# Kernel tuning notes

Measured on AMD Instinct MI355X. Metric: run time of the kernel, lower is better.

## Reference

```python
import jax, jax.numpy as jnp
import numpy as np

B, DIM_IN, DIM_OUT = 8192, 2048, 512


def setup_inputs() -> dict:
    key = jax.random.key(0)
    k1, k2, k3, k4, k5 = jax.random.split(key, 5)
    s_in = 1.0 / np.sqrt(DIM_IN)
    return {
        "x": jax.random.normal(k1, (B, DIM_IN), dtype=jnp.float32),
        "W_hazard": jax.random.normal(k2, (DIM_OUT, DIM_IN), dtype=jnp.float32) * s_in,
        "b_hazard": jax.random.normal(k3, (DIM_OUT,), dtype=jnp.float32) * s_in,
        "W_base": jax.random.normal(k4, (1, DIM_IN), dtype=jnp.float32) * s_in,
        "b_base": jax.random.normal(k5, (1,), dtype=jnp.float32) * s_in,
    }


def reference(x, W_hazard, b_hazard, W_base, b_base):
    # hazards = ReLU(x @ W_h^T + b_h)  -> [B, T]
    hazards = jax.nn.relu(jnp.einsum("bd,td->bt", x, W_hazard) + b_hazard)
    # Triangular-mask expand+sum is exactly an inclusive prefix sum along T:
    # cum_prob[b, j] = sum_{i <= j} hazards[b, i] + base_hazard[b]
    cum_hazards = jnp.cumsum(hazards, axis=1)
    base_hazard = jnp.einsum("bd,od->bo", x, W_base) + b_base  # [B, 1]
    return cum_hazards + base_hazard
```

## Files before the change

kernel.cpp:

```cpp
#include <hip/hip_runtime.h>
#include <hip/hip_bf16.h>


typedef __attribute__((ext_vector_type(8))) short  short8;
typedef __attribute__((ext_vector_type(4))) short  short4v;
typedef __attribute__((ext_vector_type(4))) float  float4v;
typedef __attribute__((ext_vector_type(4))) float  f32x4;

#define DIN  2048
#define DOUT 512
#define NROW 8192
#define BM   32
#define NPH  (DIN / 64)

static __device__ __forceinline__ unsigned short f2bf(float f) {
  union { float f; unsigned int u; } v; v.f = f;
  unsigned int u = v.u;
  unsigned int r = (u + 0x7FFFu + ((u >> 16) & 1u)) >> 16;
  return (unsigned short)r;
}

static __device__ __forceinline__ void barrier_nd() {
  asm volatile("s_waitcnt lgkmcnt(0)" ::: "memory");
  __builtin_amdgcn_s_barrier();
}

__global__ __launch_bounds__(256) void k_pack(const float* __restrict__ W,
                                              unsigned short* __restrict__ Wp) {
  int t    = blockIdx.x * 256 + threadIdx.x;
  int lane = t & 63;
  int frag = t >> 6;
  int nt   = frag >> 6, ktp = frag & 63;
  int n = nt * 16 + (lane & 15);
  int k = ktp * 32 + (lane >> 4) * 8;
  const float* src = W + (size_t)n * DIN + k;
  float4v a = __builtin_nontemporal_load((const float4v*)src);
  float4v b = __builtin_nontemporal_load((const float4v*)(src + 4));
  unsigned short o[8] = { f2bf(a.x), f2bf(a.y), f2bf(a.z), f2bf(a.w),
                          f2bf(b.x), f2bf(b.y), f2bf(b.z), f2bf(b.w) };
  *(short8*)(Wp + (size_t)t * 8) = *(const short8*)o;
}

__global__ __launch_bounds__(1024, 4) void k_main(
    const float* __restrict__ x, const unsigned short* __restrict__ Wp,
    const float* __restrict__ b_h, const float* __restrict__ w_base,
    const float* __restrict__ b_base, float* __restrict__ out) {
  __shared__ unsigned short Asw[2][BM * 64];
  __shared__ float WbL[DIN];
  __shared__ float stripT[BM][16];
  __shared__ float baseL[BM];

  const int tid  = threadIdx.x;
  const int lane = tid & 63;
  const int w    = tid >> 6;
  const int q    = lane >> 4;
  const int lm   = lane & 15;
  const int m0   = blockIdx.x * BM;
  const bool stager = (tid < 512);

  const int sr  = tid >> 4;
  const int seg = tid & 15;
  const int sOff = (sr & 31) * 64 + (((seg >> 1) ^ (sr & 7)) << 3) + (seg & 1) * 4;

  for (int i = tid; i < DIN; i += 1024) WbL[i] = w_base[i];

  f32x4 acc[2][2];
  const f32x4 z4 = {0.f, 0.f, 0.f, 0.f};
#pragma unroll
  for (int mi = 0; mi < 2; ++mi)
#pragma unroll
    for (int ni = 0; ni < 2; ++ni) acc[mi][ni] = z4;

  float4v a0, a1;
  short8  wf0[2][2], wf1[2][2];
  float   basePart = 0.f;

  auto loadA = [&](float4v& A, int kt) {
    if (stager)
      A = __builtin_nontemporal_load(
          (const float4v*)(x + (size_t)(m0 + sr) * DIN + kt * 64 + seg * 4));
  };
  auto loadB = [&](short8 wf[2][2], int kt) {
#pragma unroll
    for (int ni = 0; ni < 2; ++ni)
#pragma unroll
      for (int h = 0; h < 2; ++h) {
        int frag = (w * 2 + ni) * 64 + (kt * 2 + h);
        wf[ni][h] = *(const short8*)(Wp + ((size_t)frag << 9) + lane * 8);
      }
  };
  auto writeA = [&](unsigned short* As, const float4v& A, int kt) {
    if (stager) {
      unsigned short t4[4] = { f2bf(A.x), f2bf(A.y), f2bf(A.z), f2bf(A.w) };
      *(short4v*)&As[sOff] = *(const short4v*)t4;
      float4v wb = *(const float4v*)&WbL[kt * 64 + seg * 4];
      basePart += A.x * wb.x + A.y * wb.y + A.z * wb.z + A.w * wb.w;
    }
  };
  auto compute = [&](const unsigned short* As, const short8 wf[2][2]) {
#pragma unroll
    for (int h = 0; h < 2; ++h) {
      short8 xf[2];
#pragma unroll
      for (int mi = 0; mi < 2; ++mi) {
        int r = mi * 16 + lm;
        int g = q + 4 * h;
        xf[mi] = *(const short8*)&As[r * 64 + ((g ^ (r & 7)) << 3)];
      }
#pragma unroll
      for (int mi = 0; mi < 2; ++mi)
#pragma unroll
        for (int ni = 0; ni < 2; ++ni)
          acc[mi][ni] = __builtin_amdgcn_mfma_f32_16x16x32_bf16(
              wf[ni][h], xf[mi], acc[mi][ni], 0, 0, 0);
    }
  };

  loadA(a0, 0); loadB(wf0, 0);
  loadA(a1, 1); loadB(wf1, 1);
  barrier_nd();
  writeA(Asw[0], a0, 0);
  barrier_nd();

  for (int kt = 0; kt < NPH; kt += 2) {
    if (kt + 2 < NPH) loadA(a0, kt + 2);
    compute(Asw[0], wf0);
    if (kt + 2 < NPH) loadB(wf0, kt + 2);
    writeA(Asw[1], a1, kt + 1);
    barrier_nd();
    if (kt + 3 < NPH) loadA(a1, kt + 3);
    compute(Asw[1], wf1);
    if (kt + 3 < NPH) loadB(wf1, kt + 3);
    if (kt + 2 < NPH) writeA(Asw[0], a0, kt + 2);
    barrier_nd();
  }

  if (stager) {
    float s = basePart;
    s += __shfl_xor(s, 1); s += __shfl_xor(s, 2);
    s += __shfl_xor(s, 4); s += __shfl_xor(s, 8);
    if (seg == 0) baseL[sr] = s + b_base[0];
  }

  float runp[2][2][4];
  float Eq[2][2];
  float niPre[2][2];
  float Tst[2];
#pragma unroll
  for (int mi = 0; mi < 2; ++mi) {
    float run = 0.f;
#pragma unroll
    for (int ni = 0; ni < 2; ++ni) {
      float4v b4 = *(const float4v*)(b_h + w * 32 + ni * 16 + q * 4);
      f32x4 v = acc[mi][ni];
      float h0 = fmaxf(v.x + b4.x, 0.f);
      float h1 = fmaxf(v.y + b4.y, 0.f);
      float h2 = fmaxf(v.z + b4.z, 0.f);
      float h3 = fmaxf(v.w + b4.w, 0.f);
      runp[mi][ni][0] = h0;
      runp[mi][ni][1] = h0 + h1;
      runp[mi][ni][2] = h0 + h1 + h2;
      runp[mi][ni][3] = h0 + h1 + h2 + h3;
      float S = runp[mi][ni][3];
      float u1 = __shfl_up(S, 16);
      float u2 = __shfl_up(S, 32);
      float u3 = __shfl_up(S, 48);
      Eq[mi][ni] = (q >= 1 ? u1 : 0.f) + (q >= 2 ? u2 : 0.f) + (q >= 3 ? u3 : 0.f);
      float G = S + __shfl_xor(S, 16);
      G += __shfl_xor(G, 32);
      niPre[mi][ni] = run;
      run += G;
    }
    Tst[mi] = run;
  }
  if (q == 0) {
#pragma unroll
    for (int mi = 0; mi < 2; ++mi) stripT[mi * 16 + lm][w] = Tst[mi];
  }
  barrier_nd();

#pragma unroll
  for (int mi = 0; mi < 2; ++mi) {
    const int row = mi * 16 + lm;
    float c = baseL[row];
#pragma unroll
    for (int j4 = 0; j4 < 4; ++j4) {
      float4v s = *(const float4v*)&stripT[row][j4 * 4];
      c += (w > j4 * 4 + 0 ? s.x : 0.f) + (w > j4 * 4 + 1 ? s.y : 0.f) +
           (w > j4 * 4 + 2 ? s.z : 0.f) + (w > j4 * 4 + 3 ? s.w : 0.f);
    }
#pragma unroll
    for (int ni = 0; ni < 2; ++ni) {
      float base = c + niPre[mi][ni] + Eq[mi][ni];
      float4v o = { runp[mi][ni][0] + base, runp[mi][ni][1] + base,
                    runp[mi][ni][2] + base, runp[mi][ni][3] + base };
      __builtin_nontemporal_store(
          o, (float4v*)(out + (size_t)(m0 + row) * DOUT + w * 32 + ni * 16 + q * 4));
    }
  }
}

extern "C" void kernel_launch(void* const* d_in, const int* in_sizes, int n_in,
                              void* d_out, int out_size, void* d_ws, size_t ws_size,
                              hipStream_t stream) {
  const float* x   = (const float*)d_in[0];
  const float* Wh  = (const float*)d_in[1];
  const float* bh  = (const float*)d_in[2];
  const float* Wb0 = (const float*)d_in[3];
  const float* bb  = (const float*)d_in[4];
  float* out = (float*)d_out;

  unsigned short* Wp = (unsigned short*)d_ws;

  k_pack<<<dim3((DOUT * DIN) / (256 * 8)), dim3(256), 0, stream>>>(Wh, Wp);
  k_main<<<dim3(NROW / BM), dim3(1024), 0, stream>>>(x, Wp, bh, Wb0, bb, out);
}
```

Measured before the change: 44.74 us.

## Retile main kernel to 64x256 blocks with carry fix-up pass for prefix sum

Each block now computes a 64-row by 256-column output tile instead of 32 rows by all 512 columns, with 16 waves laid out 2x8 and all 1024 threads staging A. The left half's row totals are written to a workspace carry array, and a new k_fix kernel adds that carry to the right half of each output row to finish the cumulative sum. The aim is better reuse of W fragments per loaded x tile and full use of threads for staging. In exchange, every x tile is now loaded and converted by two blocks, the right half of the output is read and rewritten by an extra kernel launch, and the occupancy hint drops to 2.

```diff
diff --git a/kernel.cpp b/kernel.cpp
--- a/kernel.cpp
+++ b/kernel.cpp
@@ -10,7 +10,8 @@
 #define DIN  2048
 #define DOUT 512
 #define NROW 8192
-#define BM   32
+#define BM   64
+#define BN   256
 #define NPH  (DIN / 64)
 
 static __device__ __forceinline__ unsigned short f2bf(float f) {
@@ -41,26 +42,31 @@
   *(short8*)(Wp + (size_t)t * 8) = *(const short8*)o;
 }
 
-__global__ __launch_bounds__(1024, 4) void k_main(
+__global__ __launch_bounds__(1024, 2) void k_main(
     const float* __restrict__ x, const unsigned short* __restrict__ Wp,
     const float* __restrict__ b_h, const float* __restrict__ w_base,
-    const float* __restrict__ b_base, float* __restrict__ out) {
+    const float* __restrict__ b_base, float* __restrict__ out,
+    float* __restrict__ carryG) {
   __shared__ unsigned short Asw[2][BM * 64];
   __shared__ float WbL[DIN];
-  __shared__ float stripT[BM][16];
+  __shared__ float stripT[BM][8];
   __shared__ float baseL[BM];
 
   const int tid  = threadIdx.x;
   const int lane = tid & 63;
   const int w    = tid >> 6;
+  const int wr   = w >> 3;
+  const int wc   = w & 7;
   const int q    = lane >> 4;
   const int lm   = lane & 15;
-  const int m0   = blockIdx.x * BM;
-  const bool stager = (tid < 512);
+  const int id   = blockIdx.x;
+  const int bi   = id >> 1, nj = id & 1;
+  const int m0   = bi * BM;
+  const bool isL = (nj == 0);
 
   const int sr  = tid >> 4;
   const int seg = tid & 15;
-  const int sOff = (sr & 31) * 64 + (((seg >> 1) ^ (sr & 7)) << 3) + (seg & 1) * 4;
+  const int sOff = sr * 64 + (((seg >> 1) ^ (sr & 7)) << 3) + (seg & 1) * 4;
 
   for (int i = tid; i < DIN; i += 1024) WbL[i] = w_base[i];
 
@@ -76,26 +82,24 @@
   float   basePart = 0.f;
 
   auto loadA = [&](float4v& A, int kt) {
-    if (stager)
-      A = __builtin_nontemporal_load(
-          (const float4v*)(x + (size_t)(m0 + sr) * DIN + kt * 64 + seg * 4));
+    A = __builtin_nontemporal_load(
+        (const float4v*)(x + (size_t)(m0 + sr) * DIN + kt * 64 + seg * 4));
   };
   auto loadB = [&](short8 wf[2][2], int kt) {
 #pragma unroll
     for (int ni = 0; ni < 2; ++ni)
 #pragma unroll
       for (int h = 0; h < 2; ++h) {
-        int frag = (w * 2 + ni) * 64 + (kt * 2 + h);
+        int nt   = nj * 16 + wc * 2 + ni;
+        int frag = nt * 64 + (kt * 2 + h);
         wf[ni][h] = *(const short8*)(Wp + ((size_t)frag << 9) + lane * 8);
       }
   };
   auto writeA = [&](unsigned short* As, const float4v& A, int kt) {
-    if (stager) {
-      unsigned short t4[4] = { f2bf(A.x), f2bf(A.y), f2bf(A.z), f2bf(A.w) };
-      *(short4v*)&As[sOff] = *(const short4v*)t4;
-      float4v wb = *(const float4v*)&WbL[kt * 64 + seg * 4];
-      basePart += A.x * wb.x + A.y * wb.y + A.z * wb.z + A.w * wb.w;
-    }
+    unsigned short t4[4] = { f2bf(A.x), f2bf(A.y), f2bf(A.z), f2bf(A.w) };
+    *(short4v*)&As[sOff] = *(const short4v*)t4;
+    float4v wb = *(const float4v*)&WbL[kt * 64 + seg * 4];
+    basePart += A.x * wb.x + A.y * wb.y + A.z * wb.z + A.w * wb.w;
   };
   auto compute = [&](const unsigned short* As, const short8 wf[2][2]) {
 #pragma unroll
@@ -103,7 +107,7 @@
       short8 xf[2];
 #pragma unroll
       for (int mi = 0; mi < 2; ++mi) {
-        int r = mi * 16 + lm;
+        int r = wr * 32 + mi * 16 + lm;
         int g = q + 4 * h;
         xf[mi] = *(const short8*)&As[r * 64 + ((g ^ (r & 7)) << 3)];
       }
@@ -135,13 +139,14 @@
     barrier_nd();
   }
 
-  if (stager) {
+  {
     float s = basePart;
     s += __shfl_xor(s, 1); s += __shfl_xor(s, 2);
     s += __shfl_xor(s, 4); s += __shfl_xor(s, 8);
     if (seg == 0) baseL[sr] = s + b_base[0];
   }
 
+  const int cb = nj * BN;
   float runp[2][2][4];
   float Eq[2][2];
   float niPre[2][2];
@@ -151,7 +156,7 @@
     float run = 0.f;
 #pragma unroll
     for (int ni = 0; ni < 2; ++ni) {
-      float4v b4 = *(const float4v*)(b_h + w * 32 + ni * 16 + q * 4);
+      float4v b4 = *(const float4v*)(b_h + cb + wc * 32 + ni * 16 + q * 4);
       f32x4 v = acc[mi][ni];
       float h0 = fmaxf(v.x + b4.x, 0.f);
       float h1 = fmaxf(v.y + b4.y, 0.f);
@@ -175,29 +180,41 @@
   }
   if (q == 0) {
 #pragma unroll
-    for (int mi = 0; mi < 2; ++mi) stripT[mi * 16 + lm][w] = Tst[mi];
+    for (int mi = 0; mi < 2; ++mi) stripT[wr * 32 + mi * 16 + lm][wc] = Tst[mi];
   }
   barrier_nd();
 
 #pragma unroll
   for (int mi = 0; mi < 2; ++mi) {
-    const int row = mi * 16 + lm;
-    float c = baseL[row];
-#pragma unroll
-    for (int j4 = 0; j4 < 4; ++j4) {
-      float4v s = *(const float4v*)&stripT[row][j4 * 4];
-      c += (w > j4 * 4 + 0 ? s.x : 0.f) + (w > j4 * 4 + 1 ? s.y : 0.f) +
-           (w > j4 * 4 + 2 ? s.z : 0.f) + (w > j4 * 4 + 3 ? s.w : 0.f);
-    }
+    const int row = wr * 32 + mi * 16 + lm;
+    float c = isL ? baseL[row] : 0.f;
+    float4v sA = *(const float4v*)&stripT[row][0];
+    float4v sB = *(const float4v*)&stripT[row][4];
+    c += (wc > 0 ? sA.x : 0.f) + (wc > 1 ? sA.y : 0.f) + (wc > 2 ? sA.z : 0.f) +
+         (wc > 3 ? sA.w : 0.f) + (wc > 4 ? sB.x : 0.f) + (wc > 5 ? sB.y : 0.f) +
+         (wc > 6 ? sB.z : 0.f);
+    if (isL && wc == 7 && q == 0) carryG[m0 + row] = c + Tst[mi];
 #pragma unroll
     for (int ni = 0; ni < 2; ++ni) {
       float base = c + niPre[mi][ni] + Eq[mi][ni];
       float4v o = { runp[mi][ni][0] + base, runp[mi][ni][1] + base,
                     runp[mi][ni][2] + base, runp[mi][ni][3] + base };
       __builtin_nontemporal_store(
-          o, (float4v*)(out + (size_t)(m0 + row) * DOUT + w * 32 + ni * 16 + q * 4));
+          o, (float4v*)(out + (size_t)(m0 + row) * DOUT + cb + wc * 32 + ni * 16 + q * 4));
     }
   }
+}
+
+__global__ __launch_bounds__(256) void k_fix(float* __restrict__ out,
+                                             const float* __restrict__ carry) {
+  int idx = blockIdx.x * 256 + threadIdx.x;
+  int row = idx >> 6;
+  int c4  = (idx & 63) * 4 + BN;
+  float cr = carry[row];
+  float4v* p = (float4v*)(out + (size_t)row * DOUT + c4);
+  float4v v = *p;
+  v.x += cr; v.y += cr; v.z += cr; v.w += cr;
+  __builtin_nontemporal_store(v, p);
 }
 
 extern "C" void kernel_launch(void* const* d_in, const int* in_sizes, int n_in,
@@ -210,8 +227,12 @@
   const float* bb  = (const float*)d_in[4];
   float* out = (float*)d_out;
 
-  unsigned short* Wp = (unsigned short*)d_ws;
+  char* ws = (char*)d_ws;
+  unsigned short* Wp = (unsigned short*)ws;
+  float* carry       = (float*)(ws + 2u * 1024 * 1024);
 
   k_pack<<<dim3((DOUT * DIN) / (256 * 8)), dim3(256), 0, stream>>>(Wh, Wp);
-  k_main<<<dim3(NROW / BM), dim3(1024), 0, stream>>>(x, Wp, bh, Wb0, bb, out);
-}
+  k_main<<<dim3((NROW / BM) * (DOUT / BN)), dim3(1024), 0, stream>>>(
+      x, Wp, bh, Wb0, bb, out, carry);
+  k_fix<<<dim3(NROW * (DOUT - BN) / 4 / 256), dim3(256), 0, stream>>>(out, carry);
+}
```

Result: slower. 64.90 us (+45.1%).
